# Kernel optimization log

Measured on AMD Instinct MI355X. Metric: run time of the kernel, lower is better.

## Reference

```python
import jax, jax.numpy as jnp
import numpy as np

N, E, G = 2048, 4096, 16
IN_DIM, HID, E_DIM, EDGE_H = 11, 128, 6, 64
EPS = 1e-5


def setup_inputs() -> dict:
    key = jax.random.key(0)
    ks = jax.random.split(key, 32)
    s = 0.1  # keep activations tame
    inp = {
        "h": jax.random.normal(ks[0], (N, IN_DIM), jnp.float32),
        "e": jax.random.normal(ks[1], (E, E_DIM), jnp.float32),
        "src": jax.random.randint(ks[2], (E,), 0, N, jnp.int32),
        "dst": jax.random.randint(ks[3], (E,), 0, N, jnp.int32),
        "node_graph": (jnp.arange(N, dtype=jnp.int32) // (N // G)),
        # layer 0 (in_dim=11 -> hid=128)
        "eW1_0": jax.random.normal(ks[4], (E_DIM, EDGE_H), jnp.float32) * s,
        "eb1_0": jax.random.normal(ks[5], (EDGE_H,), jnp.float32) * s,
        "eW2_0": jax.random.normal(ks[6], (EDGE_H, IN_DIM * HID), jnp.float32) * s,
        "eb2_0": jax.random.normal(ks[7], (IN_DIM * HID,), jnp.float32) * s,
        "bias_0": jax.random.normal(ks[8], (HID,), jnp.float32) * s,
        "gamma_0": jax.random.uniform(ks[9], (HID,), jnp.float32, 0.5, 1.5),
        "beta_0": jax.random.normal(ks[10], (HID,), jnp.float32) * s,
        "mean_0": jax.random.normal(ks[11], (HID,), jnp.float32) * s,
        "var_0": jax.random.uniform(ks[12], (HID,), jnp.float32, 0.5, 1.5),
        # layers 1..3 stacked (hid -> hid)
        "eW1": jax.random.normal(ks[13], (3, E_DIM, EDGE_H), jnp.float32) * s,
        "eb1": jax.random.normal(ks[14], (3, EDGE_H), jnp.float32) * s,
        "eW2": jax.random.normal(ks[15], (3, EDGE_H, HID * HID), jnp.float32) * s,
        "eb2": jax.random.normal(ks[16], (3, HID * HID), jnp.float32) * s,
        "bias": jax.random.normal(ks[17], (3, HID), jnp.float32) * s,
        "gamma": jax.random.uniform(ks[18], (3, HID), jnp.float32, 0.5, 1.5),
        "beta": jax.random.normal(ks[19], (3, HID), jnp.float32) * s,
        "mean": jax.random.normal(ks[20], (3, HID), jnp.float32) * s,
        "var": jax.random.uniform(ks[21], (3, HID), jnp.float32, 0.5, 1.5),
        # output BN (on mean readout)
        "g_out": jax.random.uniform(ks[22], (HID,), jnp.float32, 0.5, 1.5),
        "b_out": jax.random.normal(ks[23], (HID,), jnp.float32) * s,
        "m_out": jax.random.normal(ks[24], (HID,), jnp.float32) * s,
        "v_out": jax.random.uniform(ks[25], (HID,), jnp.float32, 0.5, 1.5),
    }
    return inp


def _bn(x, ga, be, mu, vv):
    return (x - mu) * jax.lax.rsqrt(vv + EPS) * ga + be


def _nn_layer(x, e, src, dst, W1, b1, W2, b2, bb, ga, be, mu, vv, din):
    # edge MLP -> per-edge weight matrix [E, din, HID]
    w = (jax.nn.relu(e @ W1 + b1) @ W2 + b2).reshape(E, din, HID)
    msg = jnp.einsum('ei,eio->eo', x[src], w)          # per-edge message [E, HID]
    agg = jax.ops.segment_sum(msg, dst, num_segments=N)
    deg = jax.ops.segment_sum(jnp.ones((E,), x.dtype), dst, num_segments=N)
    agg = agg / jnp.maximum(deg, 1.0)[:, None] + bb    # mean aggregation + NNConv bias
    return _bn(jax.nn.relu(agg), ga, be, mu, vv)       # relu -> BatchNorm (eval)


def reference(h, e, src, dst, node_graph, eW1_0, eb1_0, eW2_0, eb2_0, bias_0,
              gamma_0, beta_0, mean_0, var_0, eW1, eb1, eW2, eb2, bias,
              gamma, beta, mean, var, g_out, b_out, m_out, v_out):
    x = _nn_layer(h, e, src, dst, eW1_0, eb1_0, eW2_0, eb2_0, bias_0,
                  gamma_0, beta_0, mean_0, var_0, IN_DIM)
    for i in range(3):
        x = _nn_layer(x, e, src, dst, eW1[i], eb1[i], eW2[i], eb2[i], bias[i],
                      gamma[i], beta[i], mean[i], var[i], HID)
    # dropout is identity in eval mode
    cnt = jax.ops.segment_sum(jnp.ones((N,), x.dtype), node_graph, num_segments=G)
    hn = jax.ops.segment_sum(x, node_graph, num_segments=G) / cnt[:, None]
    hx = jax.ops.segment_max(x, node_graph, num_segments=G)
    hn = _bn(hn, g_out, b_out, m_out, v_out)
    return jnp.concatenate([hn, hx], axis=1)  # [G, 2*HID]
```

## Files before the change

kernel.cpp:

```cpp
#include <hip/hip_runtime.h>
#include <stdint.h>

#define N_NODES 2048
#define N_EDGES 4096
#define N_GRAPH 16
#define IN_DIM  11
#define HID     128
#define E_DIMF  6
#define EDGE_H  64
#define NSLICE  65
#define ZCOLS   (NSLICE*HID)
#define BN_EPS  1e-5f

typedef __attribute__((ext_vector_type(8))) short short8;
typedef __attribute__((ext_vector_type(4))) float f32x4;

static __device__ __forceinline__ float bf2f(unsigned short u) {
  union { float f; uint32_t i; } x; x.i = ((uint32_t)u) << 16; return x.f;
}
static __device__ __forceinline__ unsigned short f2bf(float f) {
  union { float f; uint32_t i; } x; x.f = f;
  uint32_t i = x.i;
  return (unsigned short)((i + 0x7FFFu + ((i >> 16) & 1u)) >> 16);
}

__global__ void calc_deg(const int* __restrict__ dst, float* __restrict__ deg) {
  int e = blockIdx.x * 256 + threadIdx.x;
  if (e < N_EDGES) atomicAdd(&deg[dst[e]], 1.0f);
}

template <int KP>
__global__ __launch_bounds__(256) void conv_w_t(const float* __restrict__ W2,
                                                const float* __restrict__ b2,
                                                unsigned short* __restrict__ WbT,
                                                int din) {
  __shared__ unsigned short tile[128 * 130];
  const int k = blockIdx.x;
  const float* src = (k < 64) ? (W2 + (size_t)k * din * HID) : b2;
  const int t = threadIdx.x;
  for (int j = t; j < din * HID; j += 256) {
    int i = j >> 7, o = j & 127;
    tile[i * 130 + o] = f2bf(src[j]);
  }
  __syncthreads();
  for (int j = t; j < HID * KP; j += 256) {
    int o = j / KP, i = j & (KP - 1);
    unsigned short v = (i < din) ? tile[i * 130 + o] : (unsigned short)0;
    WbT[((size_t)k * HID + o) * KP + i] = v;
  }
}

__global__ void conv_x0(const float* __restrict__ h, unsigned short* __restrict__ xb0) {
  int idx = blockIdx.x * 256 + threadIdx.x;
  if (idx >= N_NODES * 32) return;
  int n = idx >> 5, i = idx & 31;
  xb0[idx] = f2bf(i < IN_DIM ? h[n * IN_DIM + i] : 0.0f);
}

__global__ void edge_mlp(const float* __restrict__ efeat, const float* __restrict__ W1,
                         const float* __restrict__ b1, float* __restrict__ h_all) {
  int idx = blockIdx.x * 256 + threadIdx.x;
  if (idx >= N_EDGES * EDGE_H) return;
  int e = idx >> 6, k = idx & 63;
  float acc = b1[k];
#pragma unroll
  for (int j = 0; j < E_DIMF; ++j) acc += efeat[e * E_DIMF + j] * W1[j * EDGE_H + k];
  h_all[idx] = fmaxf(acc, 0.0f);
}

template <int KP, int SWZ>
__global__ __launch_bounds__(256) void gemm_z(const unsigned short* __restrict__ Xb,
                                              const unsigned short* __restrict__ WbT,
                                              unsigned short* __restrict__ Z) {
  extern __shared__ unsigned short lds[];
  unsigned short* Al = lds;
  unsigned short* Bl = lds + 128 * KP;
  const int nb = blockIdx.x;
  const int mb = blockIdx.y;
  const int t = threadIdx.x;
  const int ROWB = KP * 2;
  const int NCH = 128 * ROWB / 16;
  const unsigned short* Asrc = Xb + (size_t)mb * 128 * KP;
  const unsigned short* Bsrc = WbT + (size_t)nb * 128 * KP;
  for (int c = t; c < NCH; c += 256) {
    int off = c * 16;
    int row = off / ROWB;
    int kb = off % ROWB;
    int dsto = row * ROWB + (kb ^ ((row & SWZ) << 4));
    *(uint4*)((char*)Al + dsto) = *(const uint4*)((const char*)Asrc + off);
    *(uint4*)((char*)Bl + dsto) = *(const uint4*)((const char*)Bsrc + off);
  }
  __syncthreads();

  const int w = t >> 6, l = t & 63;
  const int wm = (w >> 1) * 64, wn = (w & 1) * 64;
  const int lr = l & 15, lh = l >> 4;
  f32x4 acc[4][4] = {};
#pragma unroll
  for (int kk = 0; kk < KP; kk += 32) {
    short8 a[4], b[4];
    const int kb = (kk + lh * 8) * 2;
#pragma unroll
    for (int mi = 0; mi < 4; ++mi) {
      int row = wm + mi * 16 + lr;
      int addr = row * ROWB + (kb ^ ((row & SWZ) << 4));
      a[mi] = *(const short8*)((const char*)Al + addr);
    }
#pragma unroll
    for (int ni = 0; ni < 4; ++ni) {
      int col = wn + ni * 16 + lr;
      int addr = col * ROWB + (kb ^ ((col & SWZ) << 4));
      b[ni] = *(const short8*)((const char*)Bl + addr);
    }
#pragma unroll
    for (int mi = 0; mi < 4; ++mi)
#pragma unroll
      for (int ni = 0; ni < 4; ++ni)
        acc[mi][ni] = __builtin_amdgcn_mfma_f32_16x16x32_bf16(a[mi], b[ni], acc[mi][ni], 0, 0, 0);
  }
#pragma unroll
  for (int mi = 0; mi < 4; ++mi) {
#pragma unroll
    for (int ni = 0; ni < 4; ++ni) {
#pragma unroll
      for (int r = 0; r < 4; ++r) {
        int grow = mb * 128 + wm + mi * 16 + lh * 4 + r;
        int gcol = nb * 128 + wn + ni * 16 + lr;
        Z[(size_t)grow * ZCOLS + gcol] = f2bf(acc[mi][ni][r]);
      }
    }
  }
}

__global__ __launch_bounds__(128) void contract_agg(
    const float* __restrict__ h_all, const unsigned short* __restrict__ Z,
    const int* __restrict__ src, const int* __restrict__ dst,
    float* __restrict__ agg) {
  int e = blockIdx.x;
  int t = threadIdx.x;
  __shared__ float hs[NSLICE];
  if (t <= 64) hs[t] = (t < 64) ? h_all[e * EDGE_H + t] : 1.0f;
  __syncthreads();
  int s = src[e], d = dst[e];
  const unsigned short* zr = Z + (size_t)s * ZCOLS;
  float acc = 0.0f;
  for (int k = 0; k < NSLICE; ++k) acc += hs[k] * bf2f(zr[k * HID + t]);
  atomicAdd(&agg[d * HID + t], acc);
}

__global__ void finalize(const float* __restrict__ agg, const float* __restrict__ deg,
                         const float* __restrict__ bias, const float* __restrict__ gamma,
                         const float* __restrict__ beta, const float* __restrict__ mean,
                         const float* __restrict__ var, float* __restrict__ xout,
                         unsigned short* __restrict__ xbout) {
  int idx = blockIdx.x * 256 + threadIdx.x;
  if (idx >= N_NODES * HID) return;
  int n = idx >> 7, o = idx & 127;
  float v = agg[idx] / fmaxf(deg[n], 1.0f) + bias[o];
  v = fmaxf(v, 0.0f);
  v = (v - mean[o]) * rsqrtf(var[o] + BN_EPS) * gamma[o] + beta[o];
  xout[idx] = v;
  xbout[idx] = f2bf(v);
}

__global__ void readout_accum(const float* __restrict__ x, const int* __restrict__ ng,
                              float* __restrict__ gsum, unsigned int* __restrict__ gmax,
                              float* __restrict__ gcnt) {
  int idx = blockIdx.x * 256 + threadIdx.x;
  if (idx >= N_NODES * HID) return;
  int n = idx >> 7, o = idx & 127;
  int g = ng[n];
  float v = x[idx];
  atomicAdd(&gsum[g * HID + o], v);
  unsigned int u = __float_as_uint(v);
  unsigned int key = (u & 0x80000000u) ? ~u : (u | 0x80000000u);
  atomicMax(&gmax[g * HID + o], key);
  if (o == 0) atomicAdd(&gcnt[g], 1.0f);
}

__global__ void out_final(const float* __restrict__ gsum, const unsigned int* __restrict__ gmax,
                          const float* __restrict__ gcnt,
                          const float* __restrict__ g_out, const float* __restrict__ b_out,
                          const float* __restrict__ m_out, const float* __restrict__ v_out,
                          float* __restrict__ out) {
  int g = blockIdx.x, t = threadIdx.x;
  float hn = gsum[g * HID + t] / fmaxf(gcnt[g], 1.0f);
  hn = (hn - m_out[t]) * rsqrtf(v_out[t] + BN_EPS) * g_out[t] + b_out[t];
  unsigned int key = gmax[g * HID + t];
  unsigned int u = (key & 0x80000000u) ? (key ^ 0x80000000u) : ~key;
  out[g * 2 * HID + t] = hn;
  out[g * 2 * HID + HID + t] = __uint_as_float(u);
}

extern "C" void kernel_launch(void* const* d_in, const int* in_sizes, int n_in,
                              void* d_out, int out_size, void* d_ws, size_t ws_size,
                              hipStream_t stream) {
  const float* h_in   = (const float*)d_in[0];
  const float* e_in   = (const float*)d_in[1];
  const int*   src    = (const int*)d_in[2];
  const int*   dst    = (const int*)d_in[3];
  const int*   ng     = (const int*)d_in[4];
  const float* eW1_0  = (const float*)d_in[5];
  const float* eb1_0  = (const float*)d_in[6];
  const float* eW2_0  = (const float*)d_in[7];
  const float* eb2_0  = (const float*)d_in[8];
  const float* bias_0 = (const float*)d_in[9];
  const float* gamma_0= (const float*)d_in[10];
  const float* beta_0 = (const float*)d_in[11];
  const float* mean_0 = (const float*)d_in[12];
  const float* var_0  = (const float*)d_in[13];
  const float* eW1    = (const float*)d_in[14];
  const float* eb1    = (const float*)d_in[15];
  const float* eW2    = (const float*)d_in[16];
  const float* eb2    = (const float*)d_in[17];
  const float* biasL  = (const float*)d_in[18];
  const float* gammaL = (const float*)d_in[19];
  const float* betaL  = (const float*)d_in[20];
  const float* meanL  = (const float*)d_in[21];
  const float* varL   = (const float*)d_in[22];
  const float* g_out  = (const float*)d_in[23];
  const float* b_out  = (const float*)d_in[24];
  const float* m_out  = (const float*)d_in[25];
  const float* v_out  = (const float*)d_in[26];
  float* out = (float*)d_out;

  char* ws = (char*)d_ws;
  size_t off = 0;
  auto alloc = [&](size_t bytes) {
    void* p = ws + off;
    off = (off + bytes + 255) & ~(size_t)255;
    return p;
  };
  unsigned short* Z    = (unsigned short*)alloc((size_t)N_NODES * ZCOLS * 2);
  unsigned short* WbT0 = (unsigned short*)alloc((size_t)ZCOLS * 32 * 2);
  unsigned short* WbT1 = (unsigned short*)alloc((size_t)ZCOLS * 128 * 2);
  unsigned short* WbT2 = (unsigned short*)alloc((size_t)ZCOLS * 128 * 2);
  unsigned short* WbT3 = (unsigned short*)alloc((size_t)ZCOLS * 128 * 2);
  float* h_all         = (float*)alloc((size_t)N_EDGES * EDGE_H * 4);
  unsigned short* xb0  = (unsigned short*)alloc((size_t)N_NODES * 32 * 2);
  unsigned short* xb   = (unsigned short*)alloc((size_t)N_NODES * HID * 2);
  float* xcur          = (float*)alloc((size_t)N_NODES * HID * 4);
  float* agg           = (float*)alloc((size_t)N_NODES * HID * 4);
  float* deg           = (float*)alloc((size_t)N_NODES * 4);
  float* gsum          = (float*)alloc((size_t)N_GRAPH * HID * 4);
  unsigned int* gmax   = (unsigned int*)alloc((size_t)N_GRAPH * HID * 4);
  float* gcnt          = (float*)alloc((size_t)N_GRAPH * 4);

  hipMemsetAsync(deg, 0, N_NODES * 4, stream);
  hipMemsetAsync(gsum, 0, (size_t)(N_GRAPH * HID * 8 + 256 + N_GRAPH * 4), stream);
  calc_deg<<<N_EDGES / 256, 256, 0, stream>>>(dst, deg);
  conv_w_t<32><<<65, 256, 0, stream>>>(eW2_0, eb2_0, WbT0, IN_DIM);
  conv_w_t<128><<<65, 256, 0, stream>>>(eW2, eb2, WbT1, HID);
  conv_w_t<128><<<65, 256, 0, stream>>>(eW2 + 1 * 64 * (HID * HID) / 1, eb2 + 1 * (HID * HID), WbT2, HID);
  conv_w_t<128><<<65, 256, 0, stream>>>(eW2 + 2 * 64 * (HID * HID), eb2 + 2 * (HID * HID), WbT3, HID);
  conv_x0<<<(N_NODES * 32) / 256, 256, 0, stream>>>(h_in, xb0);

  edge_mlp<<<(N_EDGES * EDGE_H) / 256, 256, 0, stream>>>(e_in, eW1_0, eb1_0, h_all);
  gemm_z<32, 3><<<dim3(65, 16), 256, 2 * 128 * 32 * 2, stream>>>(xb0, WbT0, Z);
  hipMemsetAsync(agg, 0, (size_t)N_NODES * HID * 4, stream);
  contract_agg<<<N_EDGES, 128, 0, stream>>>(h_all, Z, src, dst, agg);
  finalize<<<(N_NODES * HID) / 256, 256, 0, stream>>>(agg, deg, bias_0, gamma_0, beta_0,
                                                      mean_0, var_0, xcur, xb);

  for (int l = 0; l < 3; ++l) {
    const unsigned short* W = (l == 0) ? WbT1 : (l == 1) ? WbT2 : WbT3;
    edge_mlp<<<(N_EDGES * EDGE_H) / 256, 256, 0, stream>>>(e_in, eW1 + l * E_DIMF * EDGE_H,
                                                           eb1 + l * EDGE_H, h_all);
    gemm_z<128, 7><<<dim3(65, 16), 256, 2 * 128 * 128 * 2, stream>>>(xb, W, Z);
    hipMemsetAsync(agg, 0, (size_t)N_NODES * HID * 4, stream);
    contract_agg<<<N_EDGES, 128, 0, stream>>>(h_all, Z, src, dst, agg);
    finalize<<<(N_NODES * HID) / 256, 256, 0, stream>>>(agg, deg, biasL + l * HID,
                                                        gammaL + l * HID, betaL + l * HID,
                                                        meanL + l * HID, varL + l * HID,
                                                        xcur, xb);
  }

  readout_accum<<<(N_NODES * HID) / 256, 256, 0, stream>>>(xcur, ng, gsum, gmax, gcnt);
  out_final<<<N_GRAPH, HID, 0, stream>>>(gsum, gmax, gcnt, g_out, b_out, m_out, v_out, out);
}
```

Before: 209.5 us.

## Replace atomic edge scatter with CSR node gather fusing edge MLP, finalize and readout

Builds a CSR edge list grouped by destination node (degree count, prefix sum, scatter), then replaces the per-edge contraction with atomicAdd by a per-node gather kernel. That kernel computes the edge MLP inline, accumulates messages in registers, and applies mean, bias, ReLU and BatchNorm directly. On the last layer it also performs the readout atomics. This removes the h_all, agg and xcur buffers, their memsets and the separate finalize and readout launches, and merges the three weight-conversion launches into one. The trade-off is less parallelism per block: one block per node loops serially over its in-edges, so work is unbalanced across nodes and the edge MLP is recomputed per edge inside the loop.

```diff
diff --git a/kernel.cpp b/kernel.cpp
--- a/kernel.cpp
+++ b/kernel.cpp
@@ -24,29 +24,79 @@
   return (unsigned short)((i + 0x7FFFu + ((i >> 16) & 1u)) >> 16);
 }
 
-__global__ void calc_deg(const int* __restrict__ dst, float* __restrict__ deg) {
+__global__ void calc_deg_i(const int* __restrict__ dst, int* __restrict__ degi) {
   int e = blockIdx.x * 256 + threadIdx.x;
-  if (e < N_EDGES) atomicAdd(&deg[dst[e]], 1.0f);
-}
-
-template <int KP>
-__global__ __launch_bounds__(256) void conv_w_t(const float* __restrict__ W2,
-                                                const float* __restrict__ b2,
-                                                unsigned short* __restrict__ WbT,
-                                                int din) {
+  if (e < N_EDGES) atomicAdd(&degi[dst[e]], 1);
+}
+
+__global__ __launch_bounds__(256) void build_offsets(const int* __restrict__ degi,
+                                                     int* __restrict__ roff,
+                                                     int* __restrict__ cursor) {
+  __shared__ int part[256];
+  int t = threadIdx.x;
+  int base = t * 8;
+  int loc[8];
+  int s = 0;
+#pragma unroll
+  for (int j = 0; j < 8; ++j) { loc[j] = s; s += degi[base + j]; }
+  part[t] = s;
+  __syncthreads();
+  int pre = 0;
+  for (int i = 0; i < t; ++i) pre += part[i];
+#pragma unroll
+  for (int j = 0; j < 8; ++j) {
+    int v = pre + loc[j];
+    roff[base + j] = v;
+    cursor[base + j] = v;
+  }
+  if (t == 255) roff[N_NODES] = pre + s;
+}
+
+__global__ void scatter_edges(const int* __restrict__ dst, int* __restrict__ cursor,
+                              int* __restrict__ elist) {
+  int e = blockIdx.x * 256 + threadIdx.x;
+  if (e < N_EDGES) {
+    int pos = atomicAdd(&cursor[dst[e]], 1);
+    elist[pos] = e;
+  }
+}
+
+__global__ __launch_bounds__(256) void conv_w0(const float* __restrict__ W2,
+                                               const float* __restrict__ b2,
+                                               unsigned short* __restrict__ WbT) {
   __shared__ unsigned short tile[128 * 130];
   const int k = blockIdx.x;
-  const float* src = (k < 64) ? (W2 + (size_t)k * din * HID) : b2;
+  const float* src = (k < 64) ? (W2 + (size_t)k * IN_DIM * HID) : b2;
   const int t = threadIdx.x;
-  for (int j = t; j < din * HID; j += 256) {
+  for (int j = t; j < IN_DIM * HID; j += 256) {
     int i = j >> 7, o = j & 127;
     tile[i * 130 + o] = f2bf(src[j]);
   }
   __syncthreads();
-  for (int j = t; j < HID * KP; j += 256) {
-    int o = j / KP, i = j & (KP - 1);
-    unsigned short v = (i < din) ? tile[i * 130 + o] : (unsigned short)0;
-    WbT[((size_t)k * HID + o) * KP + i] = v;
+  for (int j = t; j < HID * 32; j += 256) {
+    int o = j >> 5, i = j & 31;
+    unsigned short v = (i < IN_DIM) ? tile[i * 130 + o] : (unsigned short)0;
+    WbT[((size_t)k * HID + o) * 32 + i] = v;
+  }
+}
+
+__global__ __launch_bounds__(256) void conv_wL(const float* __restrict__ W2,
+                                               const float* __restrict__ b2,
+                                               unsigned short* __restrict__ WbT) {
+  __shared__ unsigned short tile[128 * 130];
+  const int k = blockIdx.x, l = blockIdx.y;
+  const float* src = (k < 64) ? (W2 + ((size_t)l * 64 + k) * (HID * HID))
+                              : (b2 + (size_t)l * (HID * HID));
+  unsigned short* dstp = WbT + (size_t)l * ZCOLS * HID;
+  const int t = threadIdx.x;
+  for (int j = t; j < HID * HID; j += 256) {
+    int i = j >> 7, o = j & 127;
+    tile[i * 130 + o] = f2bf(src[j]);
+  }
+  __syncthreads();
+  for (int j = t; j < HID * HID; j += 256) {
+    int o = j >> 7, i = j & 127;
+    dstp[((size_t)k * HID + o) * HID + i] = tile[i * 130 + o];
   }
 }
 
@@ -55,17 +105,6 @@
   if (idx >= N_NODES * 32) return;
   int n = idx >> 5, i = idx & 31;
   xb0[idx] = f2bf(i < IN_DIM ? h[n * IN_DIM + i] : 0.0f);
-}
-
-__global__ void edge_mlp(const float* __restrict__ efeat, const float* __restrict__ W1,
-                         const float* __restrict__ b1, float* __restrict__ h_all) {
-  int idx = blockIdx.x * 256 + threadIdx.x;
-  if (idx >= N_EDGES * EDGE_H) return;
-  int e = idx >> 6, k = idx & 63;
-  float acc = b1[k];
-#pragma unroll
-  for (int j = 0; j < E_DIMF; ++j) acc += efeat[e * E_DIMF + j] * W1[j * EDGE_H + k];
-  h_all[idx] = fmaxf(acc, 0.0f);
 }
 
 template <int KP, int SWZ>
@@ -132,50 +171,58 @@
   }
 }
 
-__global__ __launch_bounds__(128) void contract_agg(
-    const float* __restrict__ h_all, const unsigned short* __restrict__ Z,
-    const int* __restrict__ src, const int* __restrict__ dst,
-    float* __restrict__ agg) {
-  int e = blockIdx.x;
-  int t = threadIdx.x;
-  __shared__ float hs[NSLICE];
-  if (t <= 64) hs[t] = (t < 64) ? h_all[e * EDGE_H + t] : 1.0f;
-  __syncthreads();
-  int s = src[e], d = dst[e];
-  const unsigned short* zr = Z + (size_t)s * ZCOLS;
-  float acc = 0.0f;
-  for (int k = 0; k < NSLICE; ++k) acc += hs[k] * bf2f(zr[k * HID + t]);
-  atomicAdd(&agg[d * HID + t], acc);
-}
-
-__global__ void finalize(const float* __restrict__ agg, const float* __restrict__ deg,
-                         const float* __restrict__ bias, const float* __restrict__ gamma,
-                         const float* __restrict__ beta, const float* __restrict__ mean,
-                         const float* __restrict__ var, float* __restrict__ xout,
-                         unsigned short* __restrict__ xbout) {
-  int idx = blockIdx.x * 256 + threadIdx.x;
-  if (idx >= N_NODES * HID) return;
-  int n = idx >> 7, o = idx & 127;
-  float v = agg[idx] / fmaxf(deg[n], 1.0f) + bias[o];
-  v = fmaxf(v, 0.0f);
-  v = (v - mean[o]) * rsqrtf(var[o] + BN_EPS) * gamma[o] + beta[o];
-  xout[idx] = v;
-  xbout[idx] = f2bf(v);
-}
-
-__global__ void readout_accum(const float* __restrict__ x, const int* __restrict__ ng,
-                              float* __restrict__ gsum, unsigned int* __restrict__ gmax,
-                              float* __restrict__ gcnt) {
-  int idx = blockIdx.x * 256 + threadIdx.x;
-  if (idx >= N_NODES * HID) return;
-  int n = idx >> 7, o = idx & 127;
-  int g = ng[n];
-  float v = x[idx];
-  atomicAdd(&gsum[g * HID + o], v);
-  unsigned int u = __float_as_uint(v);
-  unsigned int key = (u & 0x80000000u) ? ~u : (u | 0x80000000u);
-  atomicMax(&gmax[g * HID + o], key);
-  if (o == 0) atomicAdd(&gcnt[g], 1.0f);
+template <int LAST>
+__global__ __launch_bounds__(128) void node_gather(
+    const float* __restrict__ efeat, const float* __restrict__ W1,
+    const float* __restrict__ b1, const unsigned short* __restrict__ Z,
+    const int* __restrict__ elist, const int* __restrict__ roff,
+    const int* __restrict__ src,
+    const float* __restrict__ bias, const float* __restrict__ gamma,
+    const float* __restrict__ beta, const float* __restrict__ mean,
+    const float* __restrict__ var,
+    unsigned short* __restrict__ xbout,
+    const int* __restrict__ ng, float* __restrict__ gsum,
+    unsigned int* __restrict__ gmax, float* __restrict__ gcnt) {
+  const int n = blockIdx.x, t = threadIdx.x;
+  const int start = roff[n], end = roff[n + 1];
+  __shared__ float hs[NSLICE + 1];
+  float a0 = 0.f, a1 = 0.f, a2 = 0.f, a3 = 0.f;
+  for (int idx = start; idx < end; ++idx) {
+    const int e = elist[idx];
+    if (t < EDGE_H) {
+      float a = b1[t];
+#pragma unroll
+      for (int j = 0; j < E_DIMF; ++j) a += efeat[e * E_DIMF + j] * W1[j * EDGE_H + t];
+      hs[t] = fmaxf(a, 0.f);
+    } else if (t == EDGE_H) {
+      hs[EDGE_H] = 1.f;
+    }
+    __syncthreads();
+    const unsigned short* zr = Z + (size_t)src[e] * ZCOLS;
+#pragma unroll 4
+    for (int k = 0; k < 64; k += 4) {
+      a0 += hs[k + 0] * bf2f(zr[(k + 0) * HID + t]);
+      a1 += hs[k + 1] * bf2f(zr[(k + 1) * HID + t]);
+      a2 += hs[k + 2] * bf2f(zr[(k + 2) * HID + t]);
+      a3 += hs[k + 3] * bf2f(zr[(k + 3) * HID + t]);
+    }
+    a0 += bf2f(zr[64 * HID + t]);
+    __syncthreads();
+  }
+  const int dg = end - start;
+  float v = (a0 + a1 + a2 + a3) / (float)(dg > 0 ? dg : 1) + bias[t];
+  v = fmaxf(v, 0.f);
+  v = (v - mean[t]) * rsqrtf(var[t] + BN_EPS) * gamma[t] + beta[t];
+  if (!LAST) {
+    xbout[n * HID + t] = f2bf(v);
+  } else {
+    const int g = ng[n];
+    atomicAdd(&gsum[g * HID + t], v);
+    unsigned int u = __float_as_uint(v);
+    unsigned int key = (u & 0x80000000u) ? ~u : (u | 0x80000000u);
+    atomicMax(&gmax[g * HID + t], key);
+    if (t == 0) atomicAdd(&gcnt[g], 1.f);
+  }
 }
 
 __global__ void out_final(const float* __restrict__ gsum, const unsigned int* __restrict__ gmax,
@@ -233,48 +280,46 @@
   };
   unsigned short* Z    = (unsigned short*)alloc((size_t)N_NODES * ZCOLS * 2);
   unsigned short* WbT0 = (unsigned short*)alloc((size_t)ZCOLS * 32 * 2);
-  unsigned short* WbT1 = (unsigned short*)alloc((size_t)ZCOLS * 128 * 2);
-  unsigned short* WbT2 = (unsigned short*)alloc((size_t)ZCOLS * 128 * 2);
-  unsigned short* WbT3 = (unsigned short*)alloc((size_t)ZCOLS * 128 * 2);
-  float* h_all         = (float*)alloc((size_t)N_EDGES * EDGE_H * 4);
+  unsigned short* WbTL = (unsigned short*)alloc((size_t)3 * ZCOLS * HID * 2);
   unsigned short* xb0  = (unsigned short*)alloc((size_t)N_NODES * 32 * 2);
   unsigned short* xb   = (unsigned short*)alloc((size_t)N_NODES * HID * 2);
-  float* xcur          = (float*)alloc((size_t)N_NODES * HID * 4);
-  float* agg           = (float*)alloc((size_t)N_NODES * HID * 4);
-  float* deg           = (float*)alloc((size_t)N_NODES * 4);
   float* gsum          = (float*)alloc((size_t)N_GRAPH * HID * 4);
   unsigned int* gmax   = (unsigned int*)alloc((size_t)N_GRAPH * HID * 4);
   float* gcnt          = (float*)alloc((size_t)N_GRAPH * 4);
-
-  hipMemsetAsync(deg, 0, N_NODES * 4, stream);
-  hipMemsetAsync(gsum, 0, (size_t)(N_GRAPH * HID * 8 + 256 + N_GRAPH * 4), stream);
-  calc_deg<<<N_EDGES / 256, 256, 0, stream>>>(dst, deg);
-  conv_w_t<32><<<65, 256, 0, stream>>>(eW2_0, eb2_0, WbT0, IN_DIM);
-  conv_w_t<128><<<65, 256, 0, stream>>>(eW2, eb2, WbT1, HID);
-  conv_w_t<128><<<65, 256, 0, stream>>>(eW2 + 1 * 64 * (HID * HID) / 1, eb2 + 1 * (HID * HID), WbT2, HID);
-  conv_w_t<128><<<65, 256, 0, stream>>>(eW2 + 2 * 64 * (HID * HID), eb2 + 2 * (HID * HID), WbT3, HID);
+  int*   degi          = (int*)alloc((size_t)N_NODES * 4);
+  size_t zbytes = (size_t)((char*)(degi + N_NODES) - (char*)gsum);
+  int* roff            = (int*)alloc((size_t)(N_NODES + 1) * 4);
+  int* cursor          = (int*)alloc((size_t)N_NODES * 4);
+  int* elist           = (int*)alloc((size_t)N_EDGES * 4);
+
+  hipMemsetAsync(gsum, 0, zbytes, stream);
+  calc_deg_i<<<N_EDGES / 256, 256, 0, stream>>>(dst, degi);
+  build_offsets<<<1, 256, 0, stream>>>(degi, roff, cursor);
+  scatter_edges<<<N_EDGES / 256, 256, 0, stream>>>(dst, cursor, elist);
+  conv_w0<<<65, 256, 0, stream>>>(eW2_0, eb2_0, WbT0);
+  conv_wL<<<dim3(65, 3), 256, 0, stream>>>(eW2, eb2, WbTL);
   conv_x0<<<(N_NODES * 32) / 256, 256, 0, stream>>>(h_in, xb0);
 
-  edge_mlp<<<(N_EDGES * EDGE_H) / 256, 256, 0, stream>>>(e_in, eW1_0, eb1_0, h_all);
   gemm_z<32, 3><<<dim3(65, 16), 256, 2 * 128 * 32 * 2, stream>>>(xb0, WbT0, Z);
-  hipMemsetAsync(agg, 0, (size_t)N_NODES * HID * 4, stream);
-  contract_agg<<<N_EDGES, 128, 0, stream>>>(h_all, Z, src, dst, agg);
-  finalize<<<(N_NODES * HID) / 256, 256, 0, stream>>>(agg, deg, bias_0, gamma_0, beta_0,
-                                                      mean_0, var_0, xcur, xb);
+  node_gather<0><<<N_NODES, 128, 0, stream>>>(e_in, eW1_0, eb1_0, Z, elist, roff, src,
+                                              bias_0, gamma_0, beta_0, mean_0, var_0,
+                                              xb, ng, gsum, gmax, gcnt);
 
   for (int l = 0; l < 3; ++l) {
-    const unsigned short* W = (l == 0) ? WbT1 : (l == 1) ? WbT2 : WbT3;
-    edge_mlp<<<(N_EDGES * EDGE_H) / 256, 256, 0, stream>>>(e_in, eW1 + l * E_DIMF * EDGE_H,
-                                                           eb1 + l * EDGE_H, h_all);
-    gemm_z<128, 7><<<dim3(65, 16), 256, 2 * 128 * 128 * 2, stream>>>(xb, W, Z);
-    hipMemsetAsync(agg, 0, (size_t)N_NODES * HID * 4, stream);
-    contract_agg<<<N_EDGES, 128, 0, stream>>>(h_all, Z, src, dst, agg);
-    finalize<<<(N_NODES * HID) / 256, 256, 0, stream>>>(agg, deg, biasL + l * HID,
-                                                        gammaL + l * HID, betaL + l * HID,
-                                                        meanL + l * HID, varL + l * HID,
-                                                        xcur, xb);
-  }
-
-  readout_accum<<<(N_NODES * HID) / 256, 256, 0, stream>>>(xcur, ng, gsum, gmax, gcnt);
+    gemm_z<128, 7><<<dim3(65, 16), 256, 2 * 128 * 128 * 2, stream>>>(
+        xb, WbTL + (size_t)l * ZCOLS * HID, Z);
+    if (l < 2) {
+      node_gather<0><<<N_NODES, 128, 0, stream>>>(
+          e_in, eW1 + l * E_DIMF * EDGE_H, eb1 + l * EDGE_H, Z, elist, roff, src,
+          biasL + l * HID, gammaL + l * HID, betaL + l * HID, meanL + l * HID,
+          varL + l * HID, xb, ng, gsum, gmax, gcnt);
+    } else {
+      node_gather<1><<<N_NODES, 128, 0, stream>>>(
+          e_in, eW1 + l * E_DIMF * EDGE_H, eb1 + l * EDGE_H, Z, elist, roff, src,
+          biasL + l * HID, gammaL + l * HID, betaL + l * HID, meanL + l * HID,
+          varL + l * HID, xb, ng, gsum, gmax, gcnt);
+    }
+  }
+
   out_final<<<N_GRAPH, HID, 0, stream>>>(gsum, gmax, gcnt, g_out, b_out, m_out, v_out, out);
 }
```

Measured after the change: 202.5 us. 3.4% less time.
